# Optimization experiments

Measured on AMD Instinct MI355X. Metric: run time of the kernel, lower is better.

Reference implementation:

```python
import jax, jax.numpy as jnp
import numpy as np

BN_EPS = 1e-5
NN_EPS = 1e-8


def setup_inputs() -> dict:
    key = jax.random.key(0)
    ks = jax.random.split(key, 8)
    B, N, S, D1, D2 = 8, 8192, 2048, 128, 256
    C1, C2 = 256, 128
    Cin = D1 + D2
    return {
        "xyz1": jax.random.normal(ks[0], (B, 3, N), jnp.float32),
        "xyz2": jax.random.normal(ks[1], (B, 3, S), jnp.float32),
        "points1": jax.random.normal(ks[2], (B, D1, N), jnp.float32),
        "points2": jax.random.normal(ks[3], (B, D2, S), jnp.float32),
        "w1": jax.random.normal(ks[4], (C1, Cin), jnp.float32) / np.sqrt(Cin).astype(np.float32),
        "b1": jnp.zeros((C1,), jnp.float32),
        "gamma1": jnp.ones((C1,), jnp.float32),
        "beta1": jnp.zeros((C1,), jnp.float32),
        "w2": jax.random.normal(ks[5], (C2, C1), jnp.float32) / np.sqrt(C1).astype(np.float32),
        "b2": jnp.zeros((C2,), jnp.float32),
        "gamma2": jnp.ones((C2,), jnp.float32),
        "beta2": jnp.zeros((C2,), jnp.float32),
    }


def _three_interpolate(xyz1, xyz2, points2):
    # xyz1: [B,3,N], xyz2: [B,3,S], points2: [B,D2,S] -> [B,D2,N]
    x1 = xyz1.transpose(0, 2, 1)  # [B,N,3]
    x2 = xyz2.transpose(0, 2, 1)  # [B,S,3]
    n1 = jnp.sum(x1 * x1, axis=-1)  # [B,N]
    n2 = jnp.sum(x2 * x2, axis=-1)  # [B,S]
    # squared pairwise distances [B,N,S]
    sqd = n1[:, :, None] + n2[:, None, :] - 2.0 * jnp.einsum("bnc,bsc->bns", x1, x2)
    neg_d, idx = jax.lax.top_k(-sqd, 3)  # 3 nearest neighbors
    dist = -neg_d  # [B,N,3]
    recip = 1.0 / (dist + NN_EPS)
    weight = recip / jnp.sum(recip, axis=-1, keepdims=True)  # [B,N,3]
    p2t = points2.transpose(0, 2, 1)  # [B,S,D2]
    gathered = jax.vmap(lambda p, i: p[i])(p2t, idx)  # [B,N,3,D2]
    return jnp.einsum("bnkd,bnk->bdn", gathered, weight)  # [B,D2,N]


def _conv_bn_relu(x, w, b, gamma, beta):
    # 1x1 Conv1d == channel matmul; BN in training mode (batch stats, biased var)
    x = jnp.einsum("oi,bin->bon", w, x) + b[None, :, None]
    m = jnp.mean(x, axis=(0, 2), keepdims=True)
    v = jnp.var(x, axis=(0, 2), keepdims=True)
    x = (x - m) * jax.lax.rsqrt(v + BN_EPS) * gamma[None, :, None] + beta[None, :, None]
    return jax.nn.relu(x)


def reference(xyz1, xyz2, points1, points2, w1, b1, gamma1, beta1, w2, b2, gamma2, beta2):
    interp = _three_interpolate(xyz1, xyz2, points2)  # [B,D2,N]
    x = jnp.concatenate([points1, interp], axis=1)  # [B,D1+D2,N]
    x = _conv_bn_relu(x, w1, b1, gamma1, beta1)
    x = _conv_bn_relu(x, w2, b2, gamma2, beta2)
    return x
```

## Files before the change

kernel.cpp:

```cpp
#include <hip/hip_runtime.h>
#include <stdint.h>

#define B_   8
#define N_   8192
#define S_   2048
#define D1_  128
#define D2_  256
#define CIN_ 384
#define C1_  256
#define C2_  128
#define NSUB_ 4

typedef uint16_t u16;
typedef uint32_t u32;
typedef __attribute__((ext_vector_type(8))) short bf16x8;
typedef __attribute__((ext_vector_type(4))) float f32x4;

static __device__ __forceinline__ u16 f2bf(float f){
    union { float f; u32 u; } v; v.f = f;
    u32 r = v.u + 0x7FFF + ((v.u >> 16) & 1);
    return (u16)(r >> 16);
}
static __device__ __forceinline__ float bf2f(u16 h){
    union { u32 u; float f; } v; v.u = ((u32)h) << 16;
    return v.f;
}
static __device__ __forceinline__ uint4 pack8(const u16 h[8]){
    uint4 u;
    u.x = (u32)h[0] | ((u32)h[1] << 16);
    u.y = (u32)h[2] | ((u32)h[3] << 16);
    u.z = (u32)h[4] | ((u32)h[5] << 16);
    u.w = (u32)h[6] | ((u32)h[7] << 16);
    return u;
}
#define EXT8(dst, u) { dst[0]=bf2f((u16)(u).x); dst[1]=bf2f((u16)((u).x>>16)); \
                       dst[2]=bf2f((u16)(u).y); dst[3]=bf2f((u16)((u).y>>16)); \
                       dst[4]=bf2f((u16)(u).z); dst[5]=bf2f((u16)((u).z>>16)); \
                       dst[6]=bf2f((u16)(u).w); dst[7]=bf2f((u16)((u).w>>16)); }

static __device__ __forceinline__ float med3f(float a, float b, float c){
    float d;
    asm("v_med3_f32 %0, %1, %2, %3" : "=v"(d) : "v"(a), "v"(b), "v"(c));
    return d;
}

__global__ void k_prep_w(const float* __restrict__ w1, const float* __restrict__ w2,
                         u16* __restrict__ w1bf, u16* __restrict__ w2bf){
    int i = blockIdx.x * 256 + threadIdx.x;
    if (i < C1_*CIN_) w1bf[i] = f2bf(w1[i]);
    if (i < C2_*C1_)  w2bf[i] = f2bf(w2[i]);
}

__global__ __launch_bounds__(256) void k_p2t(const float* __restrict__ p2, u16* __restrict__ p2t){
    __shared__ float t[32][33];
    int b = blockIdx.z, s0 = blockIdx.x * 32, d0 = blockIdx.y * 32;
    int tt = threadIdx.x;
    int r = tt >> 3, c4 = (tt & 7) * 4;
    const float* src = p2 + (((size_t)b*D2_ + d0 + r) * S_ + s0 + c4);
    float4 v = *(const float4*)src;
    t[r][c4+0]=v.x; t[r][c4+1]=v.y; t[r][c4+2]=v.z; t[r][c4+3]=v.w;
    __syncthreads();
    ushort4 o;
    o.x = f2bf(t[c4+0][r]); o.y = f2bf(t[c4+1][r]);
    o.z = f2bf(t[c4+2][r]); o.w = f2bf(t[c4+3][r]);
    u16* dst = p2t + (((size_t)b*S_ + s0 + r) * D2_ + d0 + c4);
    *(ushort4*)dst = o;
}

#define INSVK(sc, k) do{ \
    float t2_ = med3f(A1[k], A2[k], (sc)); \
    float t1_ = med3f(A0[k], A1[k], (sc)); \
    A0[k] = fmaxf(A0[k], (sc)); \
    A1[k] = t1_; A2[k] = t2_; \
}while(0)
#define INSL(sc, si) do{ \
    bool c0 = ((sc) > L0) || ((sc) == L0 && (si) < K0); \
    bool c1 = ((sc) > L1) || ((sc) == L1 && (si) < K1); \
    bool c2 = ((sc) > L2) || ((sc) == L2 && (si) < K2); \
    int K2n = c2 ? (c1 ? K1 : (si)) : K2; \
    int K1n = c1 ? (c0 ? K0 : (si)) : K1; \
    int K0n = c0 ? (si) : K0; \
    float T2 = med3f(L1, L2, (sc)); \
    float T1 = med3f(L0, L1, (sc)); \
    L0 = fmaxf(L0, (sc)); \
    L1 = T1; L2 = T2; K0 = K0n; K1 = K1n; K2 = K2n; \
}while(0)

__global__ __launch_bounds__(256) void k_nn(const float* __restrict__ xyz1,
                                            const float* __restrict__ xyz2,
                                            int4* __restrict__ nn_idx4, float4* __restrict__ nn_w4){
    __shared__ float4 pt[S_];
    int b = blockIdx.y;
    int t = threadIdx.x;
    const float* xb = xyz2 + (size_t)b*3*S_;
    for (int i = t; i < S_; i += 256){
        float x = xb[i], y = xb[S_ + i], z = xb[2*S_ + i];
        float hw = 0.5f*(x*x + y*y + z*z);
        pt[i] = make_float4(x, y, z, hw);
    }
    __syncthreads();
    int slot = t >> 4, seg = t & 15;
    int nbase = blockIdx.x * 64 + slot;
    const float* x1b = xyz1 + (size_t)b*3*N_;
    float px[4], py[4], pz[4], n1[4];
    #pragma unroll
    for (int k = 0; k < 4; ++k){
        int n = nbase + 16*k;
        px[k] = x1b[n]; py[k] = x1b[N_ + n]; pz[k] = x1b[2*N_ + n];
        n1[k] = px[k]*px[k] + py[k]*py[k] + pz[k]*pz[k];
    }
    float A0[4], A1[4], A2[4];
    #pragma unroll
    for (int k = 0; k < 4; ++k){ A0[k] = A1[k] = A2[k] = -3.4e38f; }
    const float4* ptq = pt + seg*128;
    const int sQ = seg * 128;

    #pragma unroll 2
    for (int j = 0; j < 128; ++j){
        int jr = (j + seg) & 127;
        float4 c = ptq[jr];
        #pragma unroll
        for (int k = 0; k < 4; ++k){
            float sc = fmaf(px[k], c.x, fmaf(py[k], c.y, fmaf(pz[k], c.z, -c.w)));
            INSVK(sc, k);
        }
    }
    #pragma unroll
    for (int m = 1; m <= 8; m <<= 1){
        #pragma unroll
        for (int k = 0; k < 4; ++k){
            float e0 = __shfl_xor(A0[k], m), e1 = __shfl_xor(A1[k], m), e2 = __shfl_xor(A2[k], m);
            INSVK(e0, k); INSVK(e1, k); INSVK(e2, k);
        }
    }

    int i0[4], i1[4], i2[4];
    #pragma unroll
    for (int k = 0; k < 4; ++k){ i0[k] = i1[k] = i2[k] = 0x7FFFFFFF; }
    for (int j = 0; j < 128; ++j){
        int jr = (j + seg) & 127;
        float4 c = ptq[jr];
        float sc[4]; bool hit = false;
        #pragma unroll
        for (int k = 0; k < 4; ++k){
            sc[k] = fmaf(px[k], c.x, fmaf(py[k], c.y, fmaf(pz[k], c.z, -c.w)));
            hit = hit || (sc[k] >= A2[k]);
        }
        if (__any(hit)){
            int sg = sQ + jr;
            #pragma unroll
            for (int k = 0; k < 4; ++k){
                i0[k] = min(i0[k], sc[k] == A0[k] ? sg : 0x7FFFFFFF);
                i1[k] = min(i1[k], sc[k] == A1[k] ? sg : 0x7FFFFFFF);
                i2[k] = min(i2[k], sc[k] == A2[k] ? sg : 0x7FFFFFFF);
            }
        }
    }
    #pragma unroll
    for (int m = 1; m <= 8; m <<= 1){
        #pragma unroll
        for (int k = 0; k < 4; ++k){
            i0[k] = min(i0[k], __shfl_xor(i0[k], m));
            i1[k] = min(i1[k], __shfl_xor(i1[k], m));
            i2[k] = min(i2[k], __shfl_xor(i2[k], m));
        }
    }

    #pragma unroll
    for (int k = 0; k < 4; ++k){
        if (A0[k] == A1[k] || A1[k] == A2[k]){
            float L0 = -3.4e38f, L1 = -3.4e38f, L2 = -3.4e38f;
            int K0 = 0x7FFFFFFF, K1 = 0x7FFFFFFF, K2 = 0x7FFFFFFF;
            for (int j = 0; j < 128; ++j){
                float4 c = ptq[j];
                float sc = fmaf(px[k], c.x, fmaf(py[k], c.y, fmaf(pz[k], c.z, -c.w)));
                INSL(sc, sQ + j);
            }
            #pragma unroll
            for (int m = 1; m <= 8; m <<= 1){
                float e0 = __shfl_xor(L0, m), e1 = __shfl_xor(L1, m), e2 = __shfl_xor(L2, m);
                int   g0 = __shfl_xor(K0, m), g1 = __shfl_xor(K1, m), g2 = __shfl_xor(K2, m);
                INSL(e0, g0); INSL(e1, g1); INSL(e2, g2);
            }
            i0[k] = K0; i1[k] = K1; i2[k] = K2;
        }
    }

    if (seg == 0){
        #pragma unroll
        for (int k = 0; k < 4; ++k){
            float d0 = fmaf(-2.f, A0[k], n1[k]);
            float d1 = fmaf(-2.f, A1[k], n1[k]);
            float d2 = fmaf(-2.f, A2[k], n1[k]);
            float r0 = 1.f/(d0+1e-8f), r1 = 1.f/(d1+1e-8f), r2 = 1.f/(d2+1e-8f);
            float inv = 1.f/(r0+r1+r2);
            size_t base = (size_t)b*N_ + nbase + 16*k;
            nn_idx4[base] = make_int4(i0[k], i1[k], i2[k], 0);
            nn_w4[base]   = make_float4(r0*inv, r1*inv, r2*inv, 0.f);
        }
    }
}

#define SWZ(nrow, kbyte)  ((((nrow)*768 + (kbyte))) ^ (((nrow)&7)<<4))
#define SWZ2(nrow, kbyte) ((((nrow)*512 + (kbyte))) ^ (((nrow)&7)<<4))

__global__ __launch_bounds__(512, 2)
void k_conv1(const u16* __restrict__ w1bf,
    const float* __restrict__ points1, const u16* __restrict__ p2t,
    const int4* __restrict__ nn_idx4, const float4* __restrict__ nn_w4,
    u16* __restrict__ y1, float* __restrict__ part1){
    __shared__ char sm[96*1024];
    int t = threadIdx.x;
    int wave = t >> 6, lane = t & 63;
    int b = blockIdx.y, n0g = blockIdx.x * 128;
    const int nlo = lane & 15, nhi = lane >> 4;
    const int g8 = t & 15, pr = t >> 4;
    const int rb = t >> 3, q8 = t & 7;

    #pragma unroll 1
    for (int sub = 0; sub < 2; ++sub){
        char* X = sm + sub*48*1024;
        float2 va2[8];
        const float* pA = points1 + ((size_t)b*D1_ + g8*8)*N_ + n0g + sub*64 + pr*2;
        #pragma unroll
        for (int j = 0; j < 8; ++j) va2[j] = *(const float2*)(pA + (size_t)j*N_);
        size_t nb = (size_t)b*N_ + n0g + sub*64 + rb;
        int4 nid = nn_idx4[nb];
        float4 nw = nn_w4[nb];
        const u16* r0 = p2t + ((size_t)b*S_ + nid.x)*D2_ + q8*32;
        const u16* r1 = p2t + ((size_t)b*S_ + nid.y)*D2_ + q8*32;
        const u16* r2 = p2t + ((size_t)b*S_ + nid.z)*D2_ + q8*32;
        uint4 uB[12];
        #pragma unroll
        for (int c = 0; c < 4; ++c){
            uB[c]   = *(const uint4*)(r0 + c*8);
            uB[4+c] = *(const uint4*)(r1 + c*8);
            uB[8+c] = *(const uint4*)(r2 + c*8);
        }
        #pragma unroll
        for (int e = 0; e < 2; ++e){
            u16 h[8];
            #pragma unroll
            for (int j = 0; j < 8; ++j) h[j] = f2bf(e ? va2[j].y : va2[j].x);
            *(uint4*)(X + SWZ(pr*2+e, g8*16)) = pack8(h);
        }
        #pragma unroll
        for (int c = 0; c < 4; ++c){
            float f0[8], f1[8], f2v[8];
            EXT8(f0, uB[c]); EXT8(f1, uB[4+c]); EXT8(f2v, uB[8+c]);
            u16 h[8];
            #pragma unroll
            for (int e = 0; e < 8; ++e)
                h[e] = f2bf(fmaf(nw.x, f0[e], fmaf(nw.y, f1[e], nw.z*f2v[e])));
            *(uint4*)(X + SWZ(rb, (128 + q8*32 + c*8)*2)) = pack8(h);
        }
    }
    __syncthreads();

    int blk = blockIdx.y * gridDim.x + blockIdx.x;
    #pragma unroll 1
    for (int pass = 0; pass < 2; ++pass){
        bf16x8 wfr[12];
        {
            const u16* wb = w1bf + ((size_t)(pass*128 + wave*16 + nlo))*CIN_ + nhi*8;
            #pragma unroll
            for (int ks = 0; ks < 12; ++ks) wfr[ks] = *(const bf16x8*)(wb + ks*32);
        }
        float s1a[4] = {0,0,0,0}, s2a[4] = {0,0,0,0};
        #pragma unroll 1
        for (int sub = 0; sub < 2; ++sub){
            char* X = sm + sub*48*1024;
            #pragma unroll 1
            for (int rowg = 0; rowg < 4; ++rowg){
                int nrow = rowg*16 + nlo;
                f32x4 acc = {0.f,0.f,0.f,0.f};
                #pragma unroll
                for (int hf = 0; hf < 2; ++hf){
                    bf16x8 xf[6];
                    #pragma unroll
                    for (int k6 = 0; k6 < 6; ++k6)
                        xf[k6] = *(const bf16x8*)(X + SWZ(nrow, (hf*6+k6)*64 + nhi*16));
                    #pragma unroll
                    for (int k6 = 0; k6 < 6; ++k6)
                        acc = __builtin_amdgcn_mfma_f32_16x16x32_bf16(wfr[hf*6+k6], xf[k6], acc, 0,0,0);
                }
                int n = n0g + sub*64 + nrow;
                u16 h[4];
                #pragma unroll
                for (int r = 0; r < 4; ++r){
                    h[r] = f2bf(acc[r]);
                    s1a[r] += acc[r]; s2a[r] += acc[r]*acc[r];
                }
                uint2 p;
                p.x = (u32)h[0] | ((u32)h[1]<<16); p.y = (u32)h[2] | ((u32)h[3]<<16);
                *(uint2*)(y1 + ((size_t)b*N_ + n)*C1_ + pass*128 + wave*16 + nhi*4) = p;
            }
        }
        #pragma unroll
        for (int r = 0; r < 4; ++r){
            float a = s1a[r], qv = s2a[r];
            #pragma unroll
            for (int m = 1; m <= 8; m <<= 1){ a += __shfl_xor(a, m); qv += __shfl_xor(qv, m); }
            if (nlo == 0){
                int ch = pass*128 + wave*16 + nhi*4 + r;
                part1[(size_t)blk*C1_ + ch] = a;
                part1[(size_t)512*C1_ + (size_t)blk*C1_ + ch] = qv;
            }
        }
    }
}

__global__ __launch_bounds__(512, 2) void k_conv2(const u16* __restrict__ w2bf,
    const u16* __restrict__ y1, const float* __restrict__ a1c1,
    u16* __restrict__ z2bf, float* __restrict__ part2){
    __shared__ char sm[64*1024];
    int t = threadIdx.x;
    int wave = t >> 6, lane = t & 63;
    int b = blockIdx.y, n0g = blockIdx.x * 256;
    const int nlo = lane & 15, nhi = lane >> 4;

    bf16x8 wfr[8];
    {
        const u16* wb = w2bf + ((size_t)(wave*16 + nlo))*C1_ + nhi*8;
        #pragma unroll
        for (int ks = 0; ks < 8; ++ks) wfr[ks] = *(const bf16x8*)(wb + ks*32);
    }

    const int r2 = t >> 4, q16 = t & 15;
    float la8[16], lc8[16];
    {
        const float* ap = a1c1 + q16*16;
        #pragma unroll
        for (int c = 0; c < 4; ++c){
            *(float4*)(la8 + c*4) = *(const float4*)(ap + c*4);
            *(float4*)(lc8 + c*4) = *(const float4*)(ap + 256 + c*4);
        }
    }

    uint4 uy[4];
    auto ISSUE_Y = [&](int s){
        const u16* yp = y1 + ((size_t)b*N_ + n0g + s*64 + r2*2)*C1_ + q16*16;
        #pragma unroll
        for (int e = 0; e < 2; ++e)
            #pragma unroll
            for (int c = 0; c < 2; ++c)
                uy[e*2+c] = *(const uint4*)(yp + (size_t)e*C1_ + c*8);
    };
    auto COMBINE = [&](char* Z){
        #pragma unroll
        for (int e = 0; e < 2; ++e)
            #pragma unroll
            for (int c = 0; c < 2; ++c){
                float f[8]; EXT8(f, uy[e*2+c]);
                u16 h[8];
                #pragma unroll
                for (int k = 0; k < 8; ++k){
                    float z = fmaf(la8[c*8+k], f[k], lc8[c*8+k]);
                    h[k] = f2bf(z > 0.f ? z : 0.f);
                }
                *(uint4*)(Z + SWZ2(r2*2+e, q16*32 + c*16)) = pack8(h);
            }
    };

    char* Zc = sm;
    char* Zn = sm + 32*1024;

    ISSUE_Y(0);
    COMBINE(Zc);
    __syncthreads();

    float s1a[4] = {0,0,0,0}, s2a[4] = {0,0,0,0};
    const int kgB = nhi*16;

    #pragma unroll 1
    for (int s = 0; s < NSUB_; ++s){
        if (s+1 < NSUB_) ISSUE_Y(s+1);
        #pragma unroll
        for (int rowg = 0; rowg < 4; ++rowg){
            int nrow = rowg*16 + nlo;
            f32x4 acc = {0.f,0.f,0.f,0.f};
            #pragma unroll
            for (int hf = 0; hf < 2; ++hf){
                bf16x8 xf[4];
                #pragma unroll
                for (int k4 = 0; k4 < 4; ++k4)
                    xf[k4] = *(const bf16x8*)(Zc + SWZ2(nrow, (hf*4+k4)*64 + kgB));
                #pragma unroll
                for (int k4 = 0; k4 < 4; ++k4)
                    acc = __builtin_amdgcn_mfma_f32_16x16x32_bf16(wfr[hf*4+k4], xf[k4], acc, 0,0,0);
            }
            int n = n0g + s*64 + nrow;
            u16 h[4];
            #pragma unroll
            for (int r = 0; r < 4; ++r){
                h[r] = f2bf(acc[r]);
                s1a[r] += acc[r]; s2a[r] += acc[r]*acc[r];
            }
            uint2 p;
            p.x = (u32)h[0] | ((u32)h[1]<<16); p.y = (u32)h[2] | ((u32)h[3]<<16);
            *(uint2*)(z2bf + ((size_t)b*N_ + n)*C2_ + wave*16 + nhi*4) = p;
        }
        if (s+1 < NSUB_) COMBINE(Zn);
        __syncthreads();
        char* tmp = Zc; Zc = Zn; Zn = tmp;
    }

    int blk = blockIdx.y * gridDim.x + blockIdx.x;
    #pragma unroll
    for (int r = 0; r < 4; ++r){
        float a = s1a[r], qv = s2a[r];
        #pragma unroll
        for (int m = 1; m <= 8; m <<= 1){ a += __shfl_xor(a, m); qv += __shfl_xor(qv, m); }
        if (nlo == 0){
            int ch = wave*16 + nhi*4 + r;
            part2[(size_t)blk*C2_ + ch] = a;
            part2[(size_t)256*C2_ + (size_t)blk*C2_ + ch] = qv;
        }
    }
}

__global__ void k_finalize(const float* __restrict__ part, int C, int NB, float count,
                           const float* __restrict__ gamma, const float* __restrict__ beta,
                           float* __restrict__ ac){
    int o = blockIdx.x, t = threadIdx.x;
    float s1 = 0.f, s2 = 0.f;
    for (int i = t; i < NB; i += 256){
        s1 += part[(size_t)i*C + o];
        s2 += part[(size_t)NB*C + (size_t)i*C + o];
    }
    #pragma unroll
    for (int m = 1; m < 64; m <<= 1){ s1 += __shfl_xor(s1, m); s2 += __shfl_xor(s2, m); }
    __shared__ float ls[8];
    int wave = t >> 6, lane = t & 63;
    if (lane == 0){ ls[wave] = s1; ls[4+wave] = s2; }
    __syncthreads();
    if (t == 0){
        s1 = ls[0]+ls[1]+ls[2]+ls[3];
        s2 = ls[4]+ls[5]+ls[6]+ls[7];
        float mean = s1 / count;
        float var  = s2 / count - mean*mean;
        float inv  = rsqrtf(var + 1e-5f);
        float a = gamma[o] * inv;
        ac[o] = a;
        ac[C + o] = beta[o] - mean*a;
    }
}

__global__ __launch_bounds__(256) void k_apply(const u16* __restrict__ z2bf,
                                               const float* __restrict__ a2c2,
                                               float* __restrict__ out){
    __shared__ float T[128][65];
    __shared__ float la[C2_], lc[C2_];
    int b = blockIdx.y, n0 = blockIdx.x * 64;
    int t = threadIdx.x;
    if (t < C2_){ la[t] = a2c2[t]; lc[t] = a2c2[C2_ + t]; }
    __syncthreads();
    int ck = t & 15, ng = t >> 4;
    #pragma unroll
    for (int g = 0; g < 4; ++g){
        int n = g*16 + ng;
        uint4 v = *(const uint4*)(z2bf + ((size_t)b*N_ + n0 + n)*C2_ + ck*8);
        float f[8]; EXT8(f, v);
        #pragma unroll
        for (int e = 0; e < 8; ++e){
            int ch = ck*8 + e;
            T[ch][n] = fmaxf(fmaf(la[ch], f[e], lc[ch]), 0.f);
        }
    }
    __syncthreads();
    #pragma unroll
    for (int g = 0; g < 8; ++g){
        int id = g*256 + t;
        int ch = id >> 4, f4 = id & 15;
        float4 o;
        o.x = T[ch][f4*4+0]; o.y = T[ch][f4*4+1];
        o.z = T[ch][f4*4+2]; o.w = T[ch][f4*4+3];
        *(float4*)(out + ((size_t)b*C2_ + ch)*N_ + n0 + f4*4) = o;
    }
}

extern "C" void kernel_launch(void* const* d_in, const int* in_sizes, int n_in,
                              void* d_out, int out_size, void* d_ws, size_t ws_size,
                              hipStream_t stream){
    const float* xyz1    = (const float*)d_in[0];
    const float* xyz2    = (const float*)d_in[1];
    const float* points1 = (const float*)d_in[2];
    const float* points2 = (const float*)d_in[3];
    const float* w1      = (const float*)d_in[4];
    const float* gamma1  = (const float*)d_in[6];
    const float* beta1   = (const float*)d_in[7];
    const float* w2      = (const float*)d_in[8];
    const float* gamma2  = (const float*)d_in[10];
    const float* beta2   = (const float*)d_in[11];
    float* outp = (float*)d_out;

    char* ws = (char*)d_ws;
    size_t off = 0;
    auto take = [&](size_t sz) -> void* {
        void* p = ws + off;
        off = (off + sz + 255) & ~(size_t)255;
        return p;
    };
    int4*   nn_idx4 = (int4*)  take((size_t)B_*N_*16);
    float4* nn_w4   = (float4*)take((size_t)B_*N_*16);
    u16*    w1bf    = (u16*)   take((size_t)C1_*CIN_*2);
    u16*    w2bf    = (u16*)   take((size_t)C2_*C1_*2);
    u16*    p2t     = (u16*)   take((size_t)B_*S_*D2_*2);
    u16*    y1      = (u16*)   take((size_t)B_*N_*C1_*2);
    u16*    z2bf    = (u16*)   take((size_t)B_*N_*C2_*2);
    float*  part1   = (float*) take((size_t)2*512*C1_*4);
    float*  part2   = (float*) take((size_t)2*256*C2_*4);
    float*  a1c1    = (float*) take((size_t)2*C1_*4);
    float*  a2c2    = (float*) take((size_t)2*C2_*4);

    hipLaunchKernelGGL(k_prep_w, dim3(384), dim3(256), 0, stream, w1, w2, w1bf, w2bf);
    hipLaunchKernelGGL(k_p2t, dim3(S_/32, D2_/32, B_), dim3(256), 0, stream, points2, p2t);
    hipLaunchKernelGGL(k_nn, dim3(N_/64, B_), dim3(256), 0, stream, xyz1, xyz2, nn_idx4, nn_w4);
    hipLaunchKernelGGL(k_conv1, dim3(N_/128, B_), dim3(512), 0, stream,
                       w1bf, points1, p2t, nn_idx4, nn_w4, y1, part1);
    hipLaunchKernelGGL(k_finalize, dim3(C1_), dim3(256), 0, stream,
                       part1, C1_, 512, (float)(B_*N_), gamma1, beta1, a1c1);
    hipLaunchKernelGGL(k_conv2, dim3(N_/256, B_), dim3(512), 0, stream,
                       w2bf, y1, a1c1, z2bf, part2);
    hipLaunchKernelGGL(k_finalize, dim3(C2_), dim3(256), 0, stream,
                       part2, C2_, 256, (float)(B_*N_), gamma2, beta2, a2c2);
    hipLaunchKernelGGL(k_apply, dim3(N_/64, B_), dim3(256), 0, stream, z2bf, a2c2, outp);
    (void)in_sizes; (void)n_in; (void)out_size; (void)ws_size; (void)d_in;
}
```

Before: 146.8 us.

## Track neighbor indices inline during top-3 scan, drop second rescan pass

The kNN kernel now carries indices alongside the top-3 scores in the main scan and in the shuffle merge, which removes the second full pass over the 2048 candidates that recovered indices by equality, along with the tie-breaking fallback loop. Each lane now reads candidates strided by 16 instead of from a contiguous rotated chunk, and the unroll goes from 2 to 8. The insert step gains compare/select work and register pressure, and tie handling changes: equal scores no longer take the lowest index, so results could differ from top_k on exact ties.

```diff
diff --git a/kernel.cpp b/kernel.cpp
--- a/kernel.cpp
+++ b/kernel.cpp
@@ -67,23 +67,17 @@
     *(ushort4*)dst = o;
 }
 
-#define INSVK(sc, k) do{ \
+#define INSIK(sc, si, k) do{ \
+    bool c0 = (sc) > A0[k]; \
+    bool c1 = (sc) > A1[k]; \
+    bool c2 = (sc) > A2[k]; \
+    I2[k] = c2 ? (c1 ? I1[k] : (si)) : I2[k]; \
+    I1[k] = c1 ? (c0 ? I0[k] : (si)) : I1[k]; \
+    I0[k] = c0 ? (si) : I0[k]; \
     float t2_ = med3f(A1[k], A2[k], (sc)); \
     float t1_ = med3f(A0[k], A1[k], (sc)); \
     A0[k] = fmaxf(A0[k], (sc)); \
     A1[k] = t1_; A2[k] = t2_; \
-}while(0)
-#define INSL(sc, si) do{ \
-    bool c0 = ((sc) > L0) || ((sc) == L0 && (si) < K0); \
-    bool c1 = ((sc) > L1) || ((sc) == L1 && (si) < K1); \
-    bool c2 = ((sc) > L2) || ((sc) == L2 && (si) < K2); \
-    int K2n = c2 ? (c1 ? K1 : (si)) : K2; \
-    int K1n = c1 ? (c0 ? K0 : (si)) : K1; \
-    int K0n = c0 ? (si) : K0; \
-    float T2 = med3f(L1, L2, (sc)); \
-    float T1 = med3f(L0, L1, (sc)); \
-    L0 = fmaxf(L0, (sc)); \
-    L1 = T1; L2 = T2; K0 = K0n; K1 = K1n; K2 = K2n; \
 }while(0)
 
 __global__ __launch_bounds__(256) void k_nn(const float* __restrict__ xyz1,
@@ -110,19 +104,22 @@
         n1[k] = px[k]*px[k] + py[k]*py[k] + pz[k]*pz[k];
     }
     float A0[4], A1[4], A2[4];
-    #pragma unroll
-    for (int k = 0; k < 4; ++k){ A0[k] = A1[k] = A2[k] = -3.4e38f; }
-    const float4* ptq = pt + seg*128;
-    const int sQ = seg * 128;
-
-    #pragma unroll 2
+    int   I0[4], I1[4], I2[4];
+    #pragma unroll
+    for (int k = 0; k < 4; ++k){
+        A0[k] = A1[k] = A2[k] = -3.4e38f;
+        I0[k] = I1[k] = I2[k] = 0;
+    }
+    const float4* ptq = pt + seg;
+
+    #pragma unroll 8
     for (int j = 0; j < 128; ++j){
-        int jr = (j + seg) & 127;
-        float4 c = ptq[jr];
+        float4 c = ptq[(size_t)j*16];
+        int sg = seg + 16*j;
         #pragma unroll
         for (int k = 0; k < 4; ++k){
             float sc = fmaf(px[k], c.x, fmaf(py[k], c.y, fmaf(pz[k], c.z, -c.w)));
-            INSVK(sc, k);
+            INSIK(sc, sg, k);
         }
     }
     #pragma unroll
@@ -130,59 +127,8 @@
         #pragma unroll
         for (int k = 0; k < 4; ++k){
             float e0 = __shfl_xor(A0[k], m), e1 = __shfl_xor(A1[k], m), e2 = __shfl_xor(A2[k], m);
-            INSVK(e0, k); INSVK(e1, k); INSVK(e2, k);
-        }
-    }
-
-    int i0[4], i1[4], i2[4];
-    #pragma unroll
-    for (int k = 0; k < 4; ++k){ i0[k] = i1[k] = i2[k] = 0x7FFFFFFF; }
-    for (int j = 0; j < 128; ++j){
-        int jr = (j + seg) & 127;
-        float4 c = ptq[jr];
-        float sc[4]; bool hit = false;
-        #pragma unroll
-        for (int k = 0; k < 4; ++k){
-            sc[k] = fmaf(px[k], c.x, fmaf(py[k], c.y, fmaf(pz[k], c.z, -c.w)));
-            hit = hit || (sc[k] >= A2[k]);
-        }
-        if (__any(hit)){
-            int sg = sQ + jr;
-            #pragma unroll
-            for (int k = 0; k < 4; ++k){
-                i0[k] = min(i0[k], sc[k] == A0[k] ? sg : 0x7FFFFFFF);
-                i1[k] = min(i1[k], sc[k] == A1[k] ? sg : 0x7FFFFFFF);
-                i2[k] = min(i2[k], sc[k] == A2[k] ? sg : 0x7FFFFFFF);
-            }
-        }
-    }
-    #pragma unroll
-    for (int m = 1; m <= 8; m <<= 1){
-        #pragma unroll
-        for (int k = 0; k < 4; ++k){
-            i0[k] = min(i0[k], __shfl_xor(i0[k], m));
-            i1[k] = min(i1[k], __shfl_xor(i1[k], m));
-            i2[k] = min(i2[k], __shfl_xor(i2[k], m));
-        }
-    }
-
-    #pragma unroll
-    for (int k = 0; k < 4; ++k){
-        if (A0[k] == A1[k] || A1[k] == A2[k]){
-            float L0 = -3.4e38f, L1 = -3.4e38f, L2 = -3.4e38f;
-            int K0 = 0x7FFFFFFF, K1 = 0x7FFFFFFF, K2 = 0x7FFFFFFF;
-            for (int j = 0; j < 128; ++j){
-                float4 c = ptq[j];
-                float sc = fmaf(px[k], c.x, fmaf(py[k], c.y, fmaf(pz[k], c.z, -c.w)));
-                INSL(sc, sQ + j);
-            }
-            #pragma unroll
-            for (int m = 1; m <= 8; m <<= 1){
-                float e0 = __shfl_xor(L0, m), e1 = __shfl_xor(L1, m), e2 = __shfl_xor(L2, m);
-                int   g0 = __shfl_xor(K0, m), g1 = __shfl_xor(K1, m), g2 = __shfl_xor(K2, m);
-                INSL(e0, g0); INSL(e1, g1); INSL(e2, g2);
-            }
-            i0[k] = K0; i1[k] = K1; i2[k] = K2;
+            int   g0 = __shfl_xor(I0[k], m), g1 = __shfl_xor(I1[k], m), g2 = __shfl_xor(I2[k], m);
+            INSIK(e0, g0, k); INSIK(e1, g1, k); INSIK(e2, g2, k);
         }
     }
 
@@ -195,7 +141,7 @@
             float r0 = 1.f/(d0+1e-8f), r1 = 1.f/(d1+1e-8f), r2 = 1.f/(d2+1e-8f);
             float inv = 1.f/(r0+r1+r2);
             size_t base = (size_t)b*N_ + nbase + 16*k;
-            nn_idx4[base] = make_int4(i0[k], i1[k], i2[k], 0);
+            nn_idx4[base] = make_int4(I0[k], I1[k], I2[k], 0);
             nn_w4[base]   = make_float4(r0*inv, r1*inv, r2*inv, 0.f);
         }
     }
```

Result: slower. 216.2 us (+47.3%).
